# Kernel optimization log

Hardware: AMD Instinct MI355X
Metric: run time of the kernel (lower is better)

Reference implementation:

```python
import jax, jax.numpy as jnp
import numpy as np

T = 2_000_000
XDIM = 32
ZDIM = 32


def setup_inputs() -> dict:
    key = jax.random.key(0)
    k1, k2, k3, k4, k5, k6 = jax.random.split(key, 6)
    return {
        "X_t": jax.random.normal(k1, (T, XDIM), dtype=jnp.float32),
        "Z_t": jax.random.normal(k2, (T, ZDIM), dtype=jnp.float32),
        "G": jax.random.uniform(k3, (), dtype=jnp.float32),  # random.uniform(0,1) init
        "eta": jax.random.normal(k4, (XDIM,), dtype=jnp.float32),
        "zeta": jax.random.normal(k5, (ZDIM,), dtype=jnp.float32),
        "gamma": jax.random.normal(k6, (ZDIM,), dtype=jnp.float32),
    }


def reference(X_t, Z_t, G, eta, zeta, gamma):
    # addSigmoid=True path: G_hat = sigmoid(G)
    G_hat = jax.nn.sigmoid(G)
    # drive signal u[t] = <Z_t[t], gamma>; theta_t = G_hat*theta_{t-1} + u[t-1], theta_0 = 0
    u = Z_t @ gamma  # [T]

    def step(theta, u_prev):
        theta = G_hat * theta + u_prev
        return theta, theta

    _, theta_tail = jax.lax.scan(step, jnp.zeros((), X_t.dtype), u[:-1])  # [T-1]
    theta = jnp.concatenate([jnp.zeros((1,), X_t.dtype), theta_tail])  # [T]
    predicted_Y = theta + X_t @ eta + Z_t @ zeta
    return predicted_Y
```

## Files before the change

kernel.cpp:

```cpp
#include <hip/hip_runtime.h>


constexpr int DIM   = 32;
constexpr int BLOCK = 256;
constexpr int K     = 8;
constexpr int CHUNK = BLOCK * K;

__device__ __forceinline__ float sigmoidf_(float x) {
    return 1.0f / (1.0f + expf(-x));
}

__global__ __launch_bounds__(BLOCK)
void dlm_phaseA(const float* __restrict__ X,
                const float* __restrict__ Z,
                const float* __restrict__ Gp,
                const float* __restrict__ eta,
                const float* __restrict__ zeta,
                const float* __restrict__ gamma,
                float* __restrict__ v_out,
                float* __restrict__ u_ws,
                float* __restrict__ aggA,
                float* __restrict__ aggB,
                int T, int store_u)
{
    const float G = sigmoidf_(Gp[0]);
    const int c   = blockIdx.x;
    const int tid = threadIdx.x;
    const int t0  = c * CHUNK + tid * K;
    const int nval = min(K, max(0, T - t0));

    const float4* gm = reinterpret_cast<const float4*>(gamma);
    const float4* zt = reinterpret_cast<const float4*>(zeta);
    const float4* et = reinterpret_cast<const float4*>(eta);
    float4 g4[8], s4[8], e4[8];
#pragma unroll
    for (int q = 0; q < 8; ++q) { g4[q] = gm[q]; s4[q] = zt[q]; e4[q] = et[q]; }

    float uu[K], vv[K];
    float a = 1.0f, b = 0.0f;
#pragma unroll
    for (int j = 0; j < K; ++j) {
        uu[j] = 0.0f; vv[j] = 0.0f;
        if (j < nval) {
            const int t = t0 + j;
            const float4* zr = reinterpret_cast<const float4*>(Z + (size_t)t * DIM);
            const float4* xr = reinterpret_cast<const float4*>(X + (size_t)t * DIM);
            float u = 0.0f, v = 0.0f;
#pragma unroll
            for (int q = 0; q < 8; ++q) {
                float4 z = zr[q];
                float4 x = xr[q];
                u += z.x*g4[q].x + z.y*g4[q].y + z.z*g4[q].z + z.w*g4[q].w;
                v += z.x*s4[q].x + z.y*s4[q].y + z.z*s4[q].z + z.w*s4[q].w
                   + x.x*e4[q].x + x.y*e4[q].y + x.z*e4[q].z + x.w*e4[q].w;
            }
            uu[j] = u; vv[j] = v;
            b = G * b + u;
            a *= G;
        }
    }

    if (nval == K) {
        float4* vp = reinterpret_cast<float4*>(v_out + t0);
        vp[0] = make_float4(vv[0], vv[1], vv[2], vv[3]);
        vp[1] = make_float4(vv[4], vv[5], vv[6], vv[7]);
        if (store_u) {
            float4* up = reinterpret_cast<float4*>(u_ws + t0);
            up[0] = make_float4(uu[0], uu[1], uu[2], uu[3]);
            up[1] = make_float4(uu[4], uu[5], uu[6], uu[7]);
        }
    } else {
        for (int j = 0; j < nval; ++j) {
            v_out[t0 + j] = vv[j];
            if (store_u) u_ws[t0 + j] = uu[j];
        }
    }

    __shared__ float as_[BLOCK], bs_[BLOCK];
    as_[tid] = a; bs_[tid] = b;
    __syncthreads();
#pragma unroll
    for (int s = 1; s < BLOCK; s <<= 1) {
        if ((tid & (2 * s - 1)) == 0) {
            float ar = as_[tid + s], br = bs_[tid + s];
            bs_[tid] = ar * bs_[tid] + br;
            as_[tid] = as_[tid] * ar;
        }
        __syncthreads();
    }
    if (tid == 0) { aggA[c] = as_[0]; aggB[c] = bs_[0]; }
}

__global__ __launch_bounds__(1024)
void dlm_phaseB(const float* __restrict__ aggA,
                const float* __restrict__ aggB,
                float* __restrict__ carry,
                int NC)
{
    __shared__ float as_[1024], bs_[1024];
    const int tid = threadIdx.x;
    float runS = 0.0f;
    for (int base = 0; base < NC; base += 1024) {
        const int idx = base + tid;
        float a = 1.0f, b = 0.0f;
        if (idx < NC) { a = aggA[idx]; b = aggB[idx]; }
        as_[tid] = a; bs_[tid] = b;
        __syncthreads();
        for (int d = 1; d < 1024; d <<= 1) {
            float pa = 1.0f, pb = 0.0f;
            if (tid >= d) { pa = as_[tid - d]; pb = bs_[tid - d]; }
            __syncthreads();
            if (tid >= d) {
                bs_[tid] = as_[tid] * pb + bs_[tid];
                as_[tid] = pa * as_[tid];
            }
            __syncthreads();
        }
        if (idx < NC) {
            float Ae = 1.0f, Be = 0.0f;
            if (tid > 0) { Ae = as_[tid - 1]; Be = bs_[tid - 1]; }
            carry[idx] = Ae * runS + Be;
        }
        const float Atile = as_[1023];
        const float Btile = bs_[1023];
        __syncthreads();
        runS = Atile * runS + Btile;
    }
}

__global__ __launch_bounds__(BLOCK)
void dlm_phaseC(const float* __restrict__ u_ws,
                const float* __restrict__ Z,
                const float* __restrict__ Gp,
                const float* __restrict__ gamma,
                const float* __restrict__ carry,
                float* __restrict__ out,
                int T, int have_u)
{
    const float G = sigmoidf_(Gp[0]);
    const int c   = blockIdx.x;
    const int tid = threadIdx.x;
    const int t0  = c * CHUNK + tid * K;
    const int nval = min(K, max(0, T - t0));

    float uu[K];
    if (have_u) {
        if (nval == K) {
            const float4* up = reinterpret_cast<const float4*>(u_ws + t0);
            float4 u0 = up[0], u1 = up[1];
            uu[0]=u0.x; uu[1]=u0.y; uu[2]=u0.z; uu[3]=u0.w;
            uu[4]=u1.x; uu[5]=u1.y; uu[6]=u1.z; uu[7]=u1.w;
        } else {
            for (int j = 0; j < K; ++j) uu[j] = (j < nval) ? u_ws[t0 + j] : 0.0f;
        }
    } else {
        const float4* gm = reinterpret_cast<const float4*>(gamma);
        float4 g4[8];
#pragma unroll
        for (int q = 0; q < 8; ++q) g4[q] = gm[q];
#pragma unroll
        for (int j = 0; j < K; ++j) {
            uu[j] = 0.0f;
            if (j < nval) {
                const float4* zr = reinterpret_cast<const float4*>(Z + (size_t)(t0 + j) * DIM);
                float u = 0.0f;
#pragma unroll
                for (int q = 0; q < 8; ++q) {
                    float4 z = zr[q];
                    u += z.x*g4[q].x + z.y*g4[q].y + z.z*g4[q].z + z.w*g4[q].w;
                }
                uu[j] = u;
            }
        }
    }

    float a = 1.0f, b = 0.0f;
#pragma unroll
    for (int j = 0; j < K; ++j) {
        if (j < nval) { b = G * b + uu[j]; a *= G; }
    }

    __shared__ float as_[BLOCK], bs_[BLOCK];
    as_[tid] = a; bs_[tid] = b;
    __syncthreads();
#pragma unroll
    for (int d = 1; d < BLOCK; d <<= 1) {
        float pa = 1.0f, pb = 0.0f;
        if (tid >= d) { pa = as_[tid - d]; pb = bs_[tid - d]; }
        __syncthreads();
        if (tid >= d) {
            bs_[tid] = as_[tid] * pb + bs_[tid];
            as_[tid] = pa * as_[tid];
        }
        __syncthreads();
    }
    float Ae = 1.0f, Be = 0.0f;
    if (tid > 0) { Ae = as_[tid - 1]; Be = bs_[tid - 1]; }
    float s = Ae * carry[c] + Be;

    if (nval == K) {
        float4* op = reinterpret_cast<float4*>(out + t0);
        float4 v0 = op[0], v1 = op[1];
        float r[K];
        const float vj[K] = { v0.x, v0.y, v0.z, v0.w, v1.x, v1.y, v1.z, v1.w };
#pragma unroll
        for (int j = 0; j < K; ++j) {
            r[j] = s + vj[j];
            s = G * s + uu[j];
        }
        op[0] = make_float4(r[0], r[1], r[2], r[3]);
        op[1] = make_float4(r[4], r[5], r[6], r[7]);
    } else {
        for (int j = 0; j < nval; ++j) {
            const int t = t0 + j;
            const float v = out[t];
            out[t] = s + v;
            s = G * s + uu[j];
        }
    }
}

extern "C" void kernel_launch(void* const* d_in, const int* in_sizes, int n_in,
                              void* d_out, int out_size, void* d_ws, size_t ws_size,
                              hipStream_t stream)
{
    const float* X     = (const float*)d_in[0];
    const float* Z     = (const float*)d_in[1];
    const float* Gp    = (const float*)d_in[2];
    const float* eta   = (const float*)d_in[3];
    const float* zeta  = (const float*)d_in[4];
    const float* gamma = (const float*)d_in[5];
    float* out = (float*)d_out;

    const int T  = out_size;
    const int NC = (T + CHUNK - 1) / CHUNK;

    const size_t Tpad = ((size_t)T + 3) & ~(size_t)3;
    const size_t need_fast = (Tpad + 3 * (size_t)NC) * sizeof(float);
    const int store_u = (ws_size >= need_fast) ? 1 : 0;

    float* u_ws;
    float* aggA;
    if (store_u) {
        u_ws = (float*)d_ws;
        aggA = u_ws + Tpad;
    } else {
        u_ws = (float*)d_ws;
        aggA = (float*)d_ws;
    }
    float* aggB  = aggA + NC;
    float* carry = aggB + NC;

    dlm_phaseA<<<NC, BLOCK, 0, stream>>>(X, Z, Gp, eta, zeta, gamma,
                                         out, u_ws, aggA, aggB, T, store_u);
    dlm_phaseB<<<1, 1024, 0, stream>>>(aggA, aggB, carry, NC);
    dlm_phaseC<<<NC, BLOCK, 0, stream>>>(u_ws, Z, Gp, gamma, carry,
                                         out, T, store_u);
}
```

Baseline: 530.3 us.

## Coalesce row loads with 8-lane cooperative dot products and wave-level scans

Result: faster. 510.9 us (-3.7%).

```diff
diff --git a/kernel.cpp b/kernel.cpp
--- a/kernel.cpp
+++ b/kernel.cpp
@@ -3,92 +3,99 @@
 
 constexpr int DIM   = 32;
 constexpr int BLOCK = 256;
-constexpr int K     = 8;
-constexpr int CHUNK = BLOCK * K;
-
-__device__ __forceinline__ float sigmoidf_(float x) {
-    return 1.0f / (1.0f + expf(-x));
+constexpr int NWAVE = 4;
+constexpr int NT    = 4;
+constexpr int TPB   = NWAVE * NT;
+
+__device__ __forceinline__ float powi_(const float gp[7], int e) {
+    float r = 1.0f;
+#pragma unroll
+    for (int b = 0; b < 7; ++b) if (e & (1 << b)) r *= gp[b];
+    return r;
+}
+
+__device__ __forceinline__ float wsum64_(float x) {
+#pragma unroll
+    for (int d = 1; d < 64; d <<= 1) x += __shfl_xor(x, d, 64);
+    return x;
 }
 
 __global__ __launch_bounds__(BLOCK)
-void dlm_phaseA(const float* __restrict__ X,
-                const float* __restrict__ Z,
-                const float* __restrict__ Gp,
-                const float* __restrict__ eta,
-                const float* __restrict__ zeta,
-                const float* __restrict__ gamma,
-                float* __restrict__ v_out,
-                float* __restrict__ u_ws,
-                float* __restrict__ aggA,
-                float* __restrict__ aggB,
-                int T, int store_u)
-{
-    const float G = sigmoidf_(Gp[0]);
-    const int c   = blockIdx.x;
-    const int tid = threadIdx.x;
-    const int t0  = c * CHUNK + tid * K;
-    const int nval = min(K, max(0, T - t0));
-
-    const float4* gm = reinterpret_cast<const float4*>(gamma);
-    const float4* zt = reinterpret_cast<const float4*>(zeta);
-    const float4* et = reinterpret_cast<const float4*>(eta);
-    float4 g4[8], s4[8], e4[8];
-#pragma unroll
-    for (int q = 0; q < 8; ++q) { g4[q] = gm[q]; s4[q] = zt[q]; e4[q] = et[q]; }
-
-    float uu[K], vv[K];
-    float a = 1.0f, b = 0.0f;
-#pragma unroll
-    for (int j = 0; j < K; ++j) {
-        uu[j] = 0.0f; vv[j] = 0.0f;
-        if (j < nval) {
-            const int t = t0 + j;
-            const float4* zr = reinterpret_cast<const float4*>(Z + (size_t)t * DIM);
-            const float4* xr = reinterpret_cast<const float4*>(X + (size_t)t * DIM);
-            float u = 0.0f, v = 0.0f;
-#pragma unroll
-            for (int q = 0; q < 8; ++q) {
-                float4 z = zr[q];
-                float4 x = xr[q];
-                u += z.x*g4[q].x + z.y*g4[q].y + z.z*g4[q].z + z.w*g4[q].w;
-                v += z.x*s4[q].x + z.y*s4[q].y + z.z*s4[q].z + z.w*s4[q].w
-                   + x.x*e4[q].x + x.y*e4[q].y + x.z*e4[q].z + x.w*e4[q].w;
-            }
-            uu[j] = u; vv[j] = v;
-            b = G * b + u;
-            a *= G;
-        }
-    }
-
-    if (nval == K) {
-        float4* vp = reinterpret_cast<float4*>(v_out + t0);
-        vp[0] = make_float4(vv[0], vv[1], vv[2], vv[3]);
-        vp[1] = make_float4(vv[4], vv[5], vv[6], vv[7]);
-        if (store_u) {
-            float4* up = reinterpret_cast<float4*>(u_ws + t0);
-            up[0] = make_float4(uu[0], uu[1], uu[2], uu[3]);
-            up[1] = make_float4(uu[4], uu[5], uu[6], uu[7]);
-        }
-    } else {
-        for (int j = 0; j < nval; ++j) {
-            v_out[t0 + j] = vv[j];
-            if (store_u) u_ws[t0 + j] = uu[j];
-        }
-    }
-
-    __shared__ float as_[BLOCK], bs_[BLOCK];
-    as_[tid] = a; bs_[tid] = b;
+void dlm_phaseA(const float* __restrict__ X, const float* __restrict__ Z,
+                const float* __restrict__ Gp, const float* __restrict__ eta,
+                const float* __restrict__ zeta, const float* __restrict__ gamma,
+                float* __restrict__ v_out, float* __restrict__ u_ws,
+                float* __restrict__ aggA, float* __restrict__ aggB,
+                int T, int tot_tiles, int store_u)
+{
+    const int tid  = threadIdx.x;
+    const int lane = tid & 63;
+    const int w    = tid >> 6;
+    const int r    = lane >> 3, p = lane & 7;
+
+    const float G = 1.0f / (1.0f + expf(-Gp[0]));
+    float gp[7]; gp[0] = G;
+#pragma unroll
+    for (int b = 1; b < 7; ++b) gp[b] = gp[b-1] * gp[b-1];
+    const float g64 = gp[6];
+    const float wp  = powi_(gp, 63 - lane);
+
+    const float4 g4  = reinterpret_cast<const float4*>(gamma)[p];
+    const float4 zt4 = reinterpret_cast<const float4*>(zeta)[p];
+    const float4 et4 = reinterpret_cast<const float4*>(eta)[p];
+
+    const int tile0 = (blockIdx.x * NWAVE + w) * NT;
+    const int ntl   = max(0, min(NT, tot_tiles - tile0));
+
+    const int src = ((lane & 7) << 3) | (lane >> 3);
+
+    float aw = 1.0f, bw = 0.0f;
+    for (int tI = 0; tI < ntl; ++tI) {
+        const int tbase = (tile0 + tI) << 6;
+        const int valid = min(64, T - tbase);
+        float ku = 0.0f, kv = 0.0f;
+#pragma unroll
+        for (int i = 0; i < 8; ++i) {
+            const int row = tbase + i * 8 + r;
+            float pu = 0.0f, pv = 0.0f;
+            if (row < T) {
+                const float4 z = reinterpret_cast<const float4*>(Z + (size_t)row * DIM)[p];
+                const float4 x = reinterpret_cast<const float4*>(X + (size_t)row * DIM)[p];
+                pu = z.x*g4.x + z.y*g4.y + z.z*g4.z + z.w*g4.w;
+                pv = z.x*zt4.x + z.y*zt4.y + z.z*zt4.z + z.w*zt4.w
+                   + x.x*et4.x + x.y*et4.y + x.z*et4.z + x.w*et4.w;
+            }
+#pragma unroll
+            for (int d = 1; d < 8; d <<= 1) {
+                pu += __shfl_xor(pu, d, 64);
+                pv += __shfl_xor(pv, d, 64);
+            }
+            if (i == p) { ku = pu; kv = pv; }
+        }
+        const float tu = __shfl(ku, src, 64);
+        const float tv = __shfl(kv, src, 64);
+        if (lane < valid) {
+            v_out[tbase + lane] = tv;
+            if (store_u) u_ws[tbase + lane] = tu;
+        }
+        float wt, atile;
+        if (valid == 64) { wt = wp; atile = g64; }
+        else { wt = (lane < valid) ? powi_(gp, valid - 1 - lane) : 0.0f;
+               atile = powi_(gp, valid); }
+        const float btile = wsum64_(wt * tu);
+        bw = atile * bw + btile;
+        aw *= atile;
+    }
+
+    __shared__ float As[NWAVE], Bs[NWAVE];
+    if (lane == 0) { As[w] = aw; Bs[w] = bw; }
     __syncthreads();
-#pragma unroll
-    for (int s = 1; s < BLOCK; s <<= 1) {
-        if ((tid & (2 * s - 1)) == 0) {
-            float ar = as_[tid + s], br = bs_[tid + s];
-            bs_[tid] = ar * bs_[tid] + br;
-            as_[tid] = as_[tid] * ar;
-        }
-        __syncthreads();
-    }
-    if (tid == 0) { aggA[c] = as_[0]; aggB[c] = bs_[0]; }
+    if (tid == 0) {
+        float A = As[0], B = Bs[0];
+#pragma unroll
+        for (int q = 1; q < NWAVE; ++q) { B = As[q] * B + Bs[q]; A *= As[q]; }
+        aggA[blockIdx.x] = A; aggB[blockIdx.x] = B;
+    }
 }
 
 __global__ __launch_bounds__(1024)
@@ -129,93 +136,91 @@
 }
 
 __global__ __launch_bounds__(BLOCK)
-void dlm_phaseC(const float* __restrict__ u_ws,
-                const float* __restrict__ Z,
-                const float* __restrict__ Gp,
-                const float* __restrict__ gamma,
-                const float* __restrict__ carry,
-                float* __restrict__ out,
-                int T, int have_u)
-{
-    const float G = sigmoidf_(Gp[0]);
-    const int c   = blockIdx.x;
-    const int tid = threadIdx.x;
-    const int t0  = c * CHUNK + tid * K;
-    const int nval = min(K, max(0, T - t0));
-
-    float uu[K];
-    if (have_u) {
-        if (nval == K) {
-            const float4* up = reinterpret_cast<const float4*>(u_ws + t0);
-            float4 u0 = up[0], u1 = up[1];
-            uu[0]=u0.x; uu[1]=u0.y; uu[2]=u0.z; uu[3]=u0.w;
-            uu[4]=u1.x; uu[5]=u1.y; uu[6]=u1.z; uu[7]=u1.w;
-        } else {
-            for (int j = 0; j < K; ++j) uu[j] = (j < nval) ? u_ws[t0 + j] : 0.0f;
-        }
-    } else {
-        const float4* gm = reinterpret_cast<const float4*>(gamma);
-        float4 g4[8];
-#pragma unroll
-        for (int q = 0; q < 8; ++q) g4[q] = gm[q];
-#pragma unroll
-        for (int j = 0; j < K; ++j) {
-            uu[j] = 0.0f;
-            if (j < nval) {
-                const float4* zr = reinterpret_cast<const float4*>(Z + (size_t)(t0 + j) * DIM);
-                float u = 0.0f;
-#pragma unroll
-                for (int q = 0; q < 8; ++q) {
-                    float4 z = zr[q];
-                    u += z.x*g4[q].x + z.y*g4[q].y + z.z*g4[q].z + z.w*g4[q].w;
+void dlm_phaseC(const float* __restrict__ u_ws, const float* __restrict__ Z,
+                const float* __restrict__ Gp, const float* __restrict__ gamma,
+                const float* __restrict__ carry, float* __restrict__ out,
+                int T, int tot_tiles, int have_u)
+{
+    const int tid  = threadIdx.x;
+    const int lane = tid & 63;
+    const int w    = tid >> 6;
+    const int r    = lane >> 3, p = lane & 7;
+
+    const float G = 1.0f / (1.0f + expf(-Gp[0]));
+    float gp[7]; gp[0] = G;
+#pragma unroll
+    for (int b = 1; b < 7; ++b) gp[b] = gp[b-1] * gp[b-1];
+    const float g64 = gp[6];
+    const float wp  = powi_(gp, 63 - lane);
+
+    const int tile0 = (blockIdx.x * NWAVE + w) * NT;
+    const int ntl   = max(0, min(NT, tot_tiles - tile0));
+    const int src   = ((lane & 7) << 3) | (lane >> 3);
+
+    float u_reg[NT];
+    float aw = 1.0f, bw = 0.0f;
+#pragma unroll
+    for (int tI = 0; tI < NT; ++tI) {
+        u_reg[tI] = 0.0f;
+        if (tI < ntl) {
+            const int tbase = (tile0 + tI) << 6;
+            const int valid = min(64, T - tbase);
+            float tu;
+            if (have_u) {
+                tu = (lane < valid) ? u_ws[tbase + lane] : 0.0f;
+            } else {
+                const float4 g4 = reinterpret_cast<const float4*>(gamma)[p];
+                float ku = 0.0f;
+#pragma unroll
+                for (int i = 0; i < 8; ++i) {
+                    const int row = tbase + i * 8 + r;
+                    float pu = 0.0f;
+                    if (row < T) {
+                        const float4 z = reinterpret_cast<const float4*>(Z + (size_t)row * DIM)[p];
+                        pu = z.x*g4.x + z.y*g4.y + z.z*g4.z + z.w*g4.w;
+                    }
+#pragma unroll
+                    for (int d = 1; d < 8; d <<= 1) pu += __shfl_xor(pu, d, 64);
+                    if (i == p) ku = pu;
                 }
-                uu[j] = u;
-            }
-        }
-    }
-
-    float a = 1.0f, b = 0.0f;
-#pragma unroll
-    for (int j = 0; j < K; ++j) {
-        if (j < nval) { b = G * b + uu[j]; a *= G; }
-    }
-
-    __shared__ float as_[BLOCK], bs_[BLOCK];
-    as_[tid] = a; bs_[tid] = b;
+                tu = __shfl(ku, src, 64);
+                if (lane >= valid) tu = 0.0f;
+            }
+            u_reg[tI] = tu;
+            float wt, atile;
+            if (valid == 64) { wt = wp; atile = g64; }
+            else { wt = (lane < valid) ? powi_(gp, valid - 1 - lane) : 0.0f;
+                   atile = powi_(gp, valid); }
+            bw = atile * bw + wsum64_(wt * tu);
+            aw *= atile;
+        }
+    }
+
+    __shared__ float As[NWAVE], Bs[NWAVE];
+    if (lane == 0) { As[w] = aw; Bs[w] = bw; }
     __syncthreads();
-#pragma unroll
-    for (int d = 1; d < BLOCK; d <<= 1) {
-        float pa = 1.0f, pb = 0.0f;
-        if (tid >= d) { pa = as_[tid - d]; pb = bs_[tid - d]; }
-        __syncthreads();
-        if (tid >= d) {
-            bs_[tid] = as_[tid] * pb + bs_[tid];
-            as_[tid] = pa * as_[tid];
-        }
-        __syncthreads();
-    }
-    float Ae = 1.0f, Be = 0.0f;
-    if (tid > 0) { Ae = as_[tid - 1]; Be = bs_[tid - 1]; }
-    float s = Ae * carry[c] + Be;
-
-    if (nval == K) {
-        float4* op = reinterpret_cast<float4*>(out + t0);
-        float4 v0 = op[0], v1 = op[1];
-        float r[K];
-        const float vj[K] = { v0.x, v0.y, v0.z, v0.w, v1.x, v1.y, v1.z, v1.w };
-#pragma unroll
-        for (int j = 0; j < K; ++j) {
-            r[j] = s + vj[j];
-            s = G * s + uu[j];
-        }
-        op[0] = make_float4(r[0], r[1], r[2], r[3]);
-        op[1] = make_float4(r[4], r[5], r[6], r[7]);
-    } else {
-        for (int j = 0; j < nval; ++j) {
-            const int t = t0 + j;
-            const float v = out[t];
-            out[t] = s + v;
-            s = G * s + uu[j];
+    float s = carry[blockIdx.x];
+    for (int q = 0; q < w; ++q) s = As[q] * s + Bs[q];
+
+#pragma unroll
+    for (int tI = 0; tI < NT; ++tI) {
+        if (tI < ntl) {
+            const int tbase = (tile0 + tI) << 6;
+            const int valid = min(64, T - tbase);
+            float A = G, B = u_reg[tI];
+#pragma unroll
+            for (int d = 1; d < 64; d <<= 1) {
+                const float Ap = __shfl_up(A, d, 64);
+                const float Bp = __shfl_up(B, d, 64);
+                if (lane >= d) { B = A * Bp + B; A = A * Ap; }
+            }
+            const float Ax = __shfl_up(A, 1, 64);
+            const float Bx = __shfl_up(B, 1, 64);
+            const float theta = (lane == 0) ? s : (Ax * s + Bx);
+            if (lane < valid) out[tbase + lane] = theta + out[tbase + lane];
+            const float A63 = __shfl(A, 63, 64);
+            const float B63 = __shfl(B, 63, 64);
+            s = A63 * s + B63;
         }
     }
 }
@@ -232,28 +237,22 @@
     const float* gamma = (const float*)d_in[5];
     float* out = (float*)d_out;
 
-    const int T  = out_size;
-    const int NC = (T + CHUNK - 1) / CHUNK;
+    const int T     = out_size;
+    const int tiles = (T + 63) >> 6;
+    const int NC    = (tiles + TPB - 1) / TPB;
 
     const size_t Tpad = ((size_t)T + 3) & ~(size_t)3;
-    const size_t need_fast = (Tpad + 3 * (size_t)NC) * sizeof(float);
-    const int store_u = (ws_size >= need_fast) ? 1 : 0;
-
-    float* u_ws;
-    float* aggA;
-    if (store_u) {
-        u_ws = (float*)d_ws;
-        aggA = u_ws + Tpad;
-    } else {
-        u_ws = (float*)d_ws;
-        aggA = (float*)d_ws;
-    }
+    const size_t need = (Tpad + 3 * (size_t)NC) * sizeof(float);
+    const int store_u = (ws_size >= need) ? 1 : 0;
+
+    float* u_ws  = (float*)d_ws;
+    float* aggA  = store_u ? (u_ws + Tpad) : (float*)d_ws;
     float* aggB  = aggA + NC;
     float* carry = aggB + NC;
 
     dlm_phaseA<<<NC, BLOCK, 0, stream>>>(X, Z, Gp, eta, zeta, gamma,
-                                         out, u_ws, aggA, aggB, T, store_u);
+                                         out, u_ws, aggA, aggB, T, tiles, store_u);
     dlm_phaseB<<<1, 1024, 0, stream>>>(aggA, aggB, carry, NC);
     dlm_phaseC<<<NC, BLOCK, 0, stream>>>(u_ws, Z, Gp, gamma, carry,
-                                         out, T, store_u);
-}
+                                         out, T, tiles, store_u);
+}
```
